# Kernel optimization log

Hardware: AMD Instinct MI355X
Metric: run time of the kernel (lower is better)

Reference implementation:

```python
import jax, jax.numpy as jnp
import numpy as np

B, C, N, K = 8, 64, 4096, 16


def setup_inputs() -> dict:
    key = jax.random.key(0)
    k1, k2 = jax.random.split(key)
    x = jax.random.normal(k1, (B, C, N, 1), dtype=jnp.float32)
    edge_index = jax.random.randint(k2, (B, N, K), 0, N, dtype=jnp.int32)
    alpha = jnp.float32(1.0)  # AlphaLayer parameter, init 1.0
    return {"x": x, "edge_index": edge_index, "alpha": alpha}


def _aggregate_sum(x_nodes, edge_index):
    # x_nodes: [B, N, C]; edge_index: [B, N, K] neighbor ids per node.
    b, n, c = x_nodes.shape
    k = edge_index.shape[-1]
    idx = edge_index.reshape(b, n * k, 1).astype(jnp.int32)
    gathered = jnp.take_along_axis(x_nodes, idx, axis=1)  # [B, N*K, C]
    return gathered.reshape(b, n, k, c).sum(axis=2)       # [B, N, C]


def reference(x, edge_index, alpha):
    # x: [B, C, N, 1] -> permute(0,2,3,1) -> [B, N, 1, C]; W=1 so treat as [B, N, C]
    x_nodes = jnp.transpose(x[..., 0], (0, 2, 1))          # [B, N, C]
    m = _aggregate_sum(x_nodes, edge_index)                # [B, N, C]
    m = jnp.transpose(m, (0, 2, 1))[..., None]             # back to [B, C, N, 1]
    # AlphaLayer: x * (1 + alpha) + m
    return x * (1.0 + alpha) + m
```

## Files before the change

### kernel.cpp

```cpp
#include <hip/hip_runtime.h>

#define B_ 8
#define C_ 64
#define N_ 4096
#define K_ 16
#define THREADS 1024
#define CG 8
#define NQ 4

__device__ __forceinline__ unsigned pack2(float lo, float hi) {
  return ((__float_as_uint(lo) + 0x8000u) >> 16) |
         ((__float_as_uint(hi) + 0x8000u) & 0xffff0000u);
}

__global__ __launch_bounds__(THREADS) void fused_k(const float* __restrict__ x,
                                                   const int* __restrict__ ei,
                                                   const float* __restrict__ alpha_p,
                                                   float* __restrict__ out) {
  __shared__ uint4 xs[N_];
  const int bid = blockIdx.x;
  const int b   = bid & 7;
  const int cg  = (bid >> 3) & 7;
  const int nq  = bid >> 6;
  const int c0  = cg * CG;
  const int t   = threadIdx.x;

  const float* xb = x + ((size_t)b * C_ + c0) * N_;

  const int node = nq * (N_ / NQ) + t;
  const int4* ep = reinterpret_cast<const int4*>(ei + ((size_t)b * N_ + node) * K_);
  const int4 e0 = ep[0], e1 = ep[1], e2 = ep[2], e3 = ep[3];

#pragma unroll
  for (int p = 0; p < N_ / THREADS; ++p) {
    const int n = p * THREADS + t;
    float r[CG];
#pragma unroll
    for (int c = 0; c < CG; ++c) r[c] = xb[c * N_ + n];
    uint4 w;
    w.x = pack2(r[0], r[1]);
    w.y = pack2(r[2], r[3]);
    w.z = pack2(r[4], r[5]);
    w.w = pack2(r[6], r[7]);
    xs[n] = w;
  }
  __syncthreads();

  int idx[K_];
  *reinterpret_cast<int4*>(&idx[0])  = e0;
  *reinterpret_cast<int4*>(&idx[4])  = e1;
  *reinterpret_cast<int4*>(&idx[8])  = e2;
  *reinterpret_cast<int4*>(&idx[12]) = e3;

  float acc[CG] = {0.f, 0.f, 0.f, 0.f, 0.f, 0.f, 0.f, 0.f};
#pragma unroll
  for (int k = 0; k < K_; ++k) {
    const uint4 v = xs[idx[k]];
    acc[0] += __uint_as_float(v.x << 16);
    acc[1] += __uint_as_float(v.x & 0xffff0000u);
    acc[2] += __uint_as_float(v.y << 16);
    acc[3] += __uint_as_float(v.y & 0xffff0000u);
    acc[4] += __uint_as_float(v.z << 16);
    acc[5] += __uint_as_float(v.z & 0xffff0000u);
    acc[6] += __uint_as_float(v.w << 16);
    acc[7] += __uint_as_float(v.w & 0xffff0000u);
  }

  const float s = 1.0f + alpha_p[0];
  float* ob = out + ((size_t)b * C_ + c0) * N_;
#pragma unroll
  for (int c = 0; c < CG; ++c) {
    ob[c * N_ + node] = xb[c * N_ + node] * s + acc[c];
  }
}

extern "C" void kernel_launch(void* const* d_in, const int* in_sizes, int n_in,
                              void* d_out, int out_size, void* d_ws, size_t ws_size,
                              hipStream_t stream) {
  const float* x     = (const float*)d_in[0];
  const int*   ei    = (const int*)d_in[1];
  const float* alpha = (const float*)d_in[2];
  float*       out   = (float*)d_out;
  (void)d_ws; (void)ws_size;

  fused_k<<<B_ * (C_ / CG) * NQ, THREADS, 0, stream>>>(x, ei, alpha, out);
}
```

Measured before the change: 11.59 us.

## Halve block size, double node split, vectorize staging loads, reuse staged self values

```diff
diff --git a/kernel.cpp b/kernel.cpp
--- a/kernel.cpp
+++ b/kernel.cpp
@@ -4,19 +4,20 @@
 #define C_ 64
 #define N_ 4096
 #define K_ 16
-#define THREADS 1024
+#define THREADS 512
 #define CG 8
-#define NQ 4
+#define NQ 8
+#define NPB (N_ / NQ)
 
 __device__ __forceinline__ unsigned pack2(float lo, float hi) {
   return ((__float_as_uint(lo) + 0x8000u) >> 16) |
          ((__float_as_uint(hi) + 0x8000u) & 0xffff0000u);
 }
 
-__global__ __launch_bounds__(THREADS) void fused_k(const float* __restrict__ x,
-                                                   const int* __restrict__ ei,
-                                                   const float* __restrict__ alpha_p,
-                                                   float* __restrict__ out) {
+__global__ __launch_bounds__(THREADS, 4) void fused_k(const float* __restrict__ x,
+                                                      const int* __restrict__ ei,
+                                                      const float* __restrict__ alpha_p,
+                                                      float* __restrict__ out) {
   __shared__ uint4 xs[N_];
   const int bid = blockIdx.x;
   const int b   = bid & 7;
@@ -27,22 +28,28 @@
 
   const float* xb = x + ((size_t)b * C_ + c0) * N_;
 
-  const int node = nq * (N_ / NQ) + t;
+  const int node = nq * NPB + t;
   const int4* ep = reinterpret_cast<const int4*>(ei + ((size_t)b * N_ + node) * K_);
   const int4 e0 = ep[0], e1 = ep[1], e2 = ep[2], e3 = ep[3];
 
 #pragma unroll
-  for (int p = 0; p < N_ / THREADS; ++p) {
-    const int n = p * THREADS + t;
-    float r[CG];
-#pragma unroll
-    for (int c = 0; c < CG; ++c) r[c] = xb[c * N_ + n];
-    uint4 w;
-    w.x = pack2(r[0], r[1]);
-    w.y = pack2(r[2], r[3]);
-    w.z = pack2(r[4], r[5]);
-    w.w = pack2(r[6], r[7]);
-    xs[n] = w;
+  for (int p = 0; p < N_ / (2 * THREADS); ++p) {
+    const int j = p * THREADS + t;
+    const float2 r0 = *reinterpret_cast<const float2*>(xb + 0 * N_ + 2 * j);
+    const float2 r1 = *reinterpret_cast<const float2*>(xb + 1 * N_ + 2 * j);
+    const float2 r2 = *reinterpret_cast<const float2*>(xb + 2 * N_ + 2 * j);
+    const float2 r3 = *reinterpret_cast<const float2*>(xb + 3 * N_ + 2 * j);
+    const float2 r4 = *reinterpret_cast<const float2*>(xb + 4 * N_ + 2 * j);
+    const float2 r5 = *reinterpret_cast<const float2*>(xb + 5 * N_ + 2 * j);
+    const float2 r6 = *reinterpret_cast<const float2*>(xb + 6 * N_ + 2 * j);
+    const float2 r7 = *reinterpret_cast<const float2*>(xb + 7 * N_ + 2 * j);
+    uint4 w0, w1;
+    w0.x = pack2(r0.x, r1.x); w0.y = pack2(r2.x, r3.x);
+    w0.z = pack2(r4.x, r5.x); w0.w = pack2(r6.x, r7.x);
+    w1.x = pack2(r0.y, r1.y); w1.y = pack2(r2.y, r3.y);
+    w1.z = pack2(r4.y, r5.y); w1.w = pack2(r6.y, r7.y);
+    xs[2 * j + 0] = w0;
+    xs[2 * j + 1] = w1;
   }
   __syncthreads();
 
@@ -66,11 +73,22 @@
     acc[7] += __uint_as_float(v.w & 0xffff0000u);
   }
 
+  const uint4 sv = xs[node];
+  float self[CG];
+  self[0] = __uint_as_float(sv.x << 16);
+  self[1] = __uint_as_float(sv.x & 0xffff0000u);
+  self[2] = __uint_as_float(sv.y << 16);
+  self[3] = __uint_as_float(sv.y & 0xffff0000u);
+  self[4] = __uint_as_float(sv.z << 16);
+  self[5] = __uint_as_float(sv.z & 0xffff0000u);
+  self[6] = __uint_as_float(sv.w << 16);
+  self[7] = __uint_as_float(sv.w & 0xffff0000u);
+
   const float s = 1.0f + alpha_p[0];
   float* ob = out + ((size_t)b * C_ + c0) * N_;
 #pragma unroll
   for (int c = 0; c < CG; ++c) {
-    ob[c * N_ + node] = xb[c * N_ + node] * s + acc[c];
+    ob[c * N_ + node] = self[c] * s + acc[c];
   }
 }
 
```

Result: slower. 13.07 us (+12.8%).
